# Optimization experiments

Hardware: AMD Instinct MI355X
Metric: run time of the kernel (lower is better)

The kernel has to match this reference:

```python
import jax, jax.numpy as jnp
import numpy as np

N, E, F_NODE, F_EDGE, H, L, G = 4096, 12288, 64, 16, 128, 4, 256
BN_EPS = 1e-5


def setup_inputs() -> dict:
    key = jax.random.key(0)
    ks = jax.random.split(key, 20)
    s = lambda k, shape, fan: jax.random.normal(k, shape, jnp.float32) * (1.0 / np.sqrt(fan))
    inp = {
        'x': jax.random.normal(ks[0], (N, F_NODE), jnp.float32),
        'edge_index': jax.random.randint(ks[1], (2, E), 0, N, dtype=jnp.int64),
        'edge_attr': jax.random.normal(ks[2], (E, F_EDGE), jnp.float32),
        'batch': jnp.sort(jax.random.randint(ks[3], (N,), 0, G, dtype=jnp.int64)),
        # node encoder
        'node_w': s(ks[4], (F_NODE, H), F_NODE),
        'node_b': jnp.zeros((H,), jnp.float32),
        # per-layer edge MLP: edge_feat -> 128 -> H*H
        'e1_w': s(ks[5], (L, F_EDGE, 128), F_EDGE),
        'e1_b': jnp.zeros((L, 128), jnp.float32),
        'e2_w': s(ks[6], (L, 128, H * H), 128) * 0.1,
        'e2_b': jnp.zeros((L, H * H), jnp.float32),
        # NNConv root weight + bias
        'root_w': s(ks[7], (L, H, H), H),
        'conv_b': jnp.zeros((L, H), jnp.float32),
        # batchnorm affine
        'bn_g': jnp.ones((L, H), jnp.float32),
        'bn_b': jnp.zeros((L, H), jnp.float32),
        # head
        'head_w1': s(ks[8], (H, H), H),
        'head_b1': jnp.zeros((H,), jnp.float32),
        'head_w2': s(ks[9], (H, 1), H),
        'head_b2': jnp.zeros((1,), jnp.float32),
    }
    return inp


def reference(x, edge_index, edge_attr, batch, node_w, node_b, e1_w, e1_b,
              e2_w, e2_b, root_w, conv_b, bn_g, bn_b, head_w1, head_b1,
              head_w2, head_b2):
    src, dst = edge_index[0], edge_index[1]
    h = x @ node_w + node_b  # [N,H]
    # in-degree for mean aggregation
    deg = jax.ops.segment_sum(jnp.ones((E,), h.dtype), dst, num_segments=N)
    inv_deg = jnp.where(deg > 0, 1.0 / jnp.maximum(deg, 1.0), 0.0)[:, None]
    for l in range(L):
        # edge MLP -> per-edge [H,H] weight
        e = jax.nn.relu(edge_attr @ e1_w[l] + e1_b[l])            # [E,128]
        W_e = (e @ e2_w[l] + e2_b[l]).reshape(E, H, H)            # [E,H,H]
        msg = jnp.einsum('eh,eho->eo', h[src], W_e)               # [E,H]
        agg = jax.ops.segment_sum(msg, dst, num_segments=N) * inv_deg
        out = agg + h @ root_w[l] + conv_b[l]
        # batchnorm (training-mode batch stats, biased var as in torch)
        mu = out.mean(0)
        var = out.var(0)
        out = (out - mu) * jax.lax.rsqrt(var + BN_EPS) * bn_g[l] + bn_b[l]
        h = h + jax.nn.relu(out)  # dropout disabled (eval)
    # global mean pool over graphs
    cnt = jax.ops.segment_sum(jnp.ones((N,), h.dtype), batch, num_segments=G)
    pooled = jax.ops.segment_sum(h, batch, num_segments=G) / jnp.maximum(cnt, 1.0)[:, None]
    y = jax.nn.relu(pooled @ head_w1 + head_b1) @ head_w2 + head_b2
    return y.squeeze(-1)  # [G]
```

## Files before the change

kernel.cpp:

```cpp
#include <hip/hip_runtime.h>

#define N_NODES 4096
#define E_TOT   12288
#define F_NODE  64
#define F_EDGE  16
#define HDIM    128
#define NLAYER  4
#define NGRAPH  256

typedef _Float16 half8 __attribute__((ext_vector_type(8)));
typedef float    f32x4 __attribute__((ext_vector_type(4)));

__global__ __launch_bounds__(256)
void k_prep_w2(const float* __restrict__ e2w, const float* __restrict__ e2b,
               _Float16* __restrict__ W2F)
{
    __shared__ _Float16 pg[16384];
    int b = blockIdx.x;
    int l = b / 129, k = b - l * 129;
    const float* src = (k < 128) ? (e2w + ((size_t)(l * 128 + k)) * 16384)
                                 : (e2b + (size_t)l * 16384);
    int t = threadIdx.x;
#pragma unroll
    for (int it = 0; it < 16; ++it) {
        int p = it * 1024 + t * 4;
        float4 v = *(const float4*)(src + p);
#pragma unroll
        for (int j4 = 0; j4 < 4; ++j4) {
            int p_ = p + j4;
            int h  = p_ >> 7, o = p_ & 127;
            int idx = ((h >> 5) * 8 + (o >> 4)) * 512
                    + (((h >> 3) & 3) * 16 + (o & 15)) * 8 + (h & 7);
            float val = (j4 == 0) ? v.x : (j4 == 1) ? v.y : (j4 == 2) ? v.z : v.w;
            pg[idx] = (_Float16)val;
        }
    }
    __syncthreads();
    _Float16* dst = W2F + (size_t)b * 16384;
#pragma unroll
    for (int it = 0; it < 8; ++it) {
        int i = it * 2048 + t * 8;
        *(half8*)(dst + i) = *(const half8*)(pg + i);
    }
}

__global__ __launch_bounds__(128)
void k_node_enc(const float* __restrict__ x, const float* __restrict__ nw,
                const float* __restrict__ nb, float* __restrict__ h,
                _Float16* __restrict__ hf)
{
    __shared__ float xl[F_NODE];
    int n = blockIdx.x, o = threadIdx.x;
    if (o < F_NODE) xl[o] = x[(size_t)n * F_NODE + o];
    __syncthreads();
    float acc = nb[o];
#pragma unroll 8
    for (int f = 0; f < F_NODE; ++f) acc += xl[f] * nw[f * HDIM + o];
    h [(size_t)n * HDIM + o] = acc;
    hf[(size_t)n * HDIM + o] = (_Float16)acc;
}

__global__ void k_deg(const int* __restrict__ dst, int* __restrict__ deg)
{
    int e = blockIdx.x * 256 + threadIdx.x;
    if (e < E_TOT) atomicAdd(&deg[dst[e]], 1);
}

__global__ void k_invd(const int* __restrict__ deg, float* __restrict__ invd)
{
    int n = blockIdx.x * 256 + threadIdx.x;
    if (n < N_NODES) invd[n] = deg[n] > 0 ? 1.0f / (float)deg[n] : 0.0f;
}

#define EF_STRIDE 136
__global__ __launch_bounds__(256)
void k_edge_mlp(const float* __restrict__ ea, const float* __restrict__ w1,
                const float* __restrict__ b1, _Float16* __restrict__ efg)
{
    __shared__ float al[16][17];
    __shared__ float wl[16][HDIM];
    __shared__ float bl[HDIM];
    int t = threadIdx.x, e0 = blockIdx.x * 16;
    if (t < HDIM) bl[t] = b1[t];
    for (int i = t; i < F_EDGE * HDIM; i += 256) wl[i >> 7][i & 127] = w1[i];
    { int i = t; al[i >> 4][i & 15] = ea[(size_t)e0 * F_EDGE + i]; }
    __syncthreads();
    int e = t >> 4, og = t & 15;
    float acc[8];
#pragma unroll
    for (int j = 0; j < 8; ++j) acc[j] = bl[og * 8 + j];
#pragma unroll
    for (int f = 0; f < F_EDGE; ++f) {
        float a = al[e][f];
#pragma unroll
        for (int j = 0; j < 8; ++j) acc[j] += a * wl[f][og * 8 + j];
    }
    half8 o;
#pragma unroll
    for (int j = 0; j < 8; ++j) o[j] = (_Float16)fmaxf(acc[j], 0.f);
    *(half8*)&efg[(size_t)(e0 + e) * EF_STRIDE + og * 8] = o;
    if (og == 0) efg[(size_t)(e0 + e) * EF_STRIDE + 128] = (_Float16)1.0f;
}

#define BM 64
#define KSPLIT 4
__global__ __launch_bounds__(128, 3)
void k_msg(const _Float16* __restrict__ W2L,
           const _Float16* __restrict__ efg,
           const _Float16* __restrict__ hf,
           const int* __restrict__ srcIdx,
           const int* __restrict__ dstIdx,
           float* __restrict__ agg,
           float* __restrict__ bns1,
           float* __restrict__ bns2)
{
    __shared__ _Float16 efs[BM][40];

    const int tid  = threadIdx.x;
    const int lane = tid & 63;
    const int w    = tid >> 6;
    const int lhi  = lane >> 4;
    const int llo  = lane & 15;

    const int bx    = blockIdx.x;
    const int code  = bx & 7;
    const int ks    = code >> 1;
    const int chH   = code & 1;
    const int tile  = bx >> 3;
    const int e0    = tile * BM;
    const int kbase = (129 * ks) >> 2;
    const int kcnt  = ((129 * (ks + 1)) >> 2) - kbase;

    if (bx == 0 && tid < HDIM) { bns1[tid] = 0.f; bns2[tid] = 0.f; }

    for (int i = tid; i < BM * 5; i += 128) {
        int r = i / 5, c = i - r * 5;
        *(half8*)&efs[r][c * 8] =
            *(const half8*)(efg + (size_t)(e0 + r) * EF_STRIDE + kbase + c * 8);
    }

    half8 hs[4][4];
#pragma unroll
    for (int rf = 0; rf < 4; ++rf) {
        int s = srcIdx[e0 + rf * 16 + llo];
        const _Float16* hp = hf + (size_t)s * HDIM + lhi * 8;
#pragma unroll
        for (int hc = 0; hc < 4; ++hc)
            hs[rf][hc] = *(const half8*)(hp + hc * 32);
    }

    __syncthreads();

    const _Float16* bp = W2L + (size_t)kbase * 16384
                             + (size_t)(chH * 4 + w * 2) * 512 + lane * 8;

#define LDQ(d0, d1, kk, hc) do {                                            \
        const _Float16* p_ = bp + (size_t)(kk) * 16384 + (hc) * 4096;       \
        d0 = *(const half8*)(p_); d1 = *(const half8*)(p_ + 512);           \
    } while (0)

    half8 b00, b01, b10, b11, b20, b21, b30, b31;
    LDQ(b00, b01, 0, 0);
    LDQ(b10, b11, 0, 1);
    LDQ(b20, b21, 0, 2);
    LDQ(b30, b31, 0, 3);

    f32x4 acc[4][2];
#pragma unroll
    for (int rf = 0; rf < 4; ++rf)
#pragma unroll
        for (int cf = 0; cf < 2; ++cf)
#pragma unroll
            for (int d = 0; d < 4; ++d) acc[rf][cf][d] = 0.f;

    for (int kk = 0; kk < kcnt; ++kk) {
        const bool nx = (kk + 1 < kcnt);
        _Float16 efv[4];
#pragma unroll
        for (int rf = 0; rf < 4; ++rf) efv[rf] = efs[rf * 16 + llo][kk];

        __builtin_amdgcn_s_setprio(1);
#pragma unroll
        for (int rf = 0; rf < 4; ++rf) {
            half8 av = hs[rf][0] * efv[rf];
            acc[rf][0] = __builtin_amdgcn_mfma_f32_16x16x32_f16(av, b00, acc[rf][0], 0, 0, 0);
            acc[rf][1] = __builtin_amdgcn_mfma_f32_16x16x32_f16(av, b01, acc[rf][1], 0, 0, 0);
        }
        if (nx) LDQ(b00, b01, kk + 1, 0);

#pragma unroll
        for (int rf = 0; rf < 4; ++rf) {
            half8 av = hs[rf][1] * efv[rf];
            acc[rf][0] = __builtin_amdgcn_mfma_f32_16x16x32_f16(av, b10, acc[rf][0], 0, 0, 0);
            acc[rf][1] = __builtin_amdgcn_mfma_f32_16x16x32_f16(av, b11, acc[rf][1], 0, 0, 0);
        }
        if (nx) LDQ(b10, b11, kk + 1, 1);

#pragma unroll
        for (int rf = 0; rf < 4; ++rf) {
            half8 av = hs[rf][2] * efv[rf];
            acc[rf][0] = __builtin_amdgcn_mfma_f32_16x16x32_f16(av, b20, acc[rf][0], 0, 0, 0);
            acc[rf][1] = __builtin_amdgcn_mfma_f32_16x16x32_f16(av, b21, acc[rf][1], 0, 0, 0);
        }
        if (nx) LDQ(b20, b21, kk + 1, 2);

#pragma unroll
        for (int rf = 0; rf < 4; ++rf) {
            half8 av = hs[rf][3] * efv[rf];
            acc[rf][0] = __builtin_amdgcn_mfma_f32_16x16x32_f16(av, b30, acc[rf][0], 0, 0, 0);
            acc[rf][1] = __builtin_amdgcn_mfma_f32_16x16x32_f16(av, b31, acc[rf][1], 0, 0, 0);
        }
        __builtin_amdgcn_s_setprio(0);
        if (nx) LDQ(b30, b31, kk + 1, 3);
    }
#undef LDQ

#pragma unroll
    for (int rf = 0; rf < 4; ++rf) {
#pragma unroll
        for (int r = 0; r < 4; ++r) {
            int row = rf * 16 + lhi * 4 + r;
            int d   = dstIdx[e0 + row];
#pragma unroll
            for (int cf = 0; cf < 2; ++cf) {
                int o = chH * 64 + w * 32 + cf * 16 + llo;
                atomicAdd(&agg[(size_t)d * HDIM + o], acc[rf][cf][r]);
            }
        }
    }
}

__global__ __launch_bounds__(128)
void k_out(const float* __restrict__ agg, const float* __restrict__ invd,
           const float* __restrict__ h, const float* __restrict__ rw,
           const float* __restrict__ cb, float* __restrict__ outb,
           float* __restrict__ bns1, float* __restrict__ bns2)
{
    __shared__ float hl[16][HDIM];
    int n0 = blockIdx.x * 16, o = threadIdx.x;
    for (int r = 0; r < 16; ++r) hl[r][o] = h[(size_t)(n0 + r) * HDIM + o];
    __syncthreads();
    float acc[16];
    float cbv = cb[o];
#pragma unroll
    for (int r = 0; r < 16; ++r)
        acc[r] = agg[(size_t)(n0 + r) * HDIM + o] * invd[n0 + r] + cbv;
    for (int hh = 0; hh < HDIM; ++hh) {
        float wv = rw[hh * HDIM + o];
#pragma unroll
        for (int r = 0; r < 16; ++r) acc[r] += hl[r][hh] * wv;
    }
    float s1 = 0.f, s2 = 0.f;
#pragma unroll
    for (int r = 0; r < 16; ++r) {
        outb[(size_t)(n0 + r) * HDIM + o] = acc[r];
        s1 += acc[r];
        s2 += acc[r] * acc[r];
    }
    atomicAdd(&bns1[o], s1);
    atomicAdd(&bns2[o], s2);
}

__global__ void k_bn_apply(const float* __restrict__ outb, const float* __restrict__ bns1,
                           const float* __restrict__ bns2, const float* __restrict__ g,
                           const float* __restrict__ b, float* __restrict__ h,
                           _Float16* __restrict__ hf, float* __restrict__ agg,
                           const int* __restrict__ batch, float* __restrict__ pooled,
                           int* __restrict__ cnt, int last)
{
    int i = blockIdx.x * 256 + threadIdx.x;
    int o = i & (HDIM - 1);
    const float inv_n = 1.0f / (float)N_NODES;
    float m   = bns1[o] * inv_n;
    float var = bns2[o] * inv_n - m * m;
    float rs  = rsqrtf(var + 1e-5f);
    float v  = (outb[i] - m) * rs * g[o] + b[o];
    float hn = h[i] + fmaxf(v, 0.f);
    h[i]  = hn;
    hf[i] = (_Float16)hn;
    if (!last) {
        agg[i] = 0.f;
    } else {
        int n  = i >> 7;
        int gg = batch[n];
        atomicAdd(&pooled[(size_t)gg * HDIM + o], hn);
        if (o == 0) atomicAdd(&cnt[gg], 1);
    }
}

__global__ __launch_bounds__(128)
void k_head(const float* __restrict__ pooled, const int* __restrict__ cnt,
            const float* __restrict__ w1, const float* __restrict__ b1,
            const float* __restrict__ w2, const float* __restrict__ b2,
            float* __restrict__ y)
{
    __shared__ float pl[HDIM];
    __shared__ float red[HDIM];
    int g = blockIdx.x, o = threadIdx.x;
    float ic = 1.0f / (float)max(cnt[g], 1);
    pl[o] = pooled[(size_t)g * HDIM + o] * ic;
    __syncthreads();
    float t = b1[o];
#pragma unroll 8
    for (int hh = 0; hh < HDIM; ++hh) t += pl[hh] * w1[hh * HDIM + o];
    t = fmaxf(t, 0.f);
    red[o] = t * w2[o];
    __syncthreads();
    for (int s = 64; s > 0; s >>= 1) {
        if (o < s) red[o] += red[o + s];
        __syncthreads();
    }
    if (o == 0) y[g] = red[0] + b2[0];
}

extern "C" void kernel_launch(void* const* d_in, const int* in_sizes, int n_in,
                              void* d_out, int out_size, void* d_ws, size_t ws_size,
                              hipStream_t stream)
{
    const float* x      = (const float*)d_in[0];
    const int*   ei     = (const int*)  d_in[1];
    const float* ea     = (const float*)d_in[2];
    const int*   batch  = (const int*)  d_in[3];
    const float* node_w = (const float*)d_in[4];
    const float* node_b = (const float*)d_in[5];
    const float* e1w    = (const float*)d_in[6];
    const float* e1b    = (const float*)d_in[7];
    const float* e2w    = (const float*)d_in[8];
    const float* e2b    = (const float*)d_in[9];
    const float* rw     = (const float*)d_in[10];
    const float* cb     = (const float*)d_in[11];
    const float* bng    = (const float*)d_in[12];
    const float* bnb    = (const float*)d_in[13];
    const float* hw1    = (const float*)d_in[14];
    const float* hb1    = (const float*)d_in[15];
    const float* hw2    = (const float*)d_in[16];
    const float* hb2    = (const float*)d_in[17];
    float* y = (float*)d_out;

    char* ws = (char*)d_ws;
    _Float16* W2F  = (_Float16*)ws; ws += 16908288;
    float*    h    = (float*)ws;    ws += 2097152;
    _Float16* hf   = (_Float16*)ws; ws += 1048576;
    _Float16* efg  = (_Float16*)ws; ws += 3342336;
    float*    agg  = (float*)ws;    ws += 2097152;
    float*    bns1 = (float*)ws;    ws += 512;
    float*    bns2 = (float*)ws;    ws += 512;
    float*    outb = (float*)ws;    ws += 2097152;
    int*      deg  = (int*)ws;      ws += 16384;
    float*    invd = (float*)ws;    ws += 16384;
    float*    pooled = (float*)ws;  ws += 131072;
    int*      cnt  = (int*)ws;      ws += 1024;

    const int* src = ei;
    const int* dst = ei + E_TOT;

    k_prep_w2<<<NLAYER * 129, 256, 0, stream>>>(e2w, e2b, W2F);
    k_node_enc<<<N_NODES, 128, 0, stream>>>(x, node_w, node_b, h, hf);
    hipMemsetAsync(deg, 0, N_NODES * sizeof(int), stream);
    k_deg<<<(E_TOT + 255) / 256, 256, 0, stream>>>(dst, deg);
    k_invd<<<(N_NODES + 255) / 256, 256, 0, stream>>>(deg, invd);
    hipMemsetAsync(agg, 0, (size_t)N_NODES * HDIM * sizeof(float), stream);
    hipMemsetAsync(pooled, 0, (size_t)NGRAPH * HDIM * sizeof(float) + NGRAPH * sizeof(int), stream);

    for (int l = 0; l < NLAYER; ++l) {
        k_edge_mlp<<<E_TOT / 16, 256, 0, stream>>>(ea, e1w + l * F_EDGE * HDIM,
                                                   e1b + l * HDIM, efg);
        k_msg<<<(E_TOT / BM) * KSPLIT * 2, 128, 0, stream>>>(
            W2F + (size_t)l * 129 * 16384, efg, hf, src, dst, agg, bns1, bns2);
        k_out<<<N_NODES / 16, 128, 0, stream>>>(agg, invd, h,
                                                rw + l * HDIM * HDIM,
                                                cb + l * HDIM, outb, bns1, bns2);
        k_bn_apply<<<(N_NODES * HDIM) / 256, 256, 0, stream>>>(
            outb, bns1, bns2, bng + l * HDIM, bnb + l * HDIM, h, hf,
            agg, batch, pooled, cnt, (l == NLAYER - 1) ? 1 : 0);
    }

    k_head<<<NGRAPH, 128, 0, stream>>>(pooled, cnt, hw1, hb1, hw2, hb2, y);
}
```

Baseline: 421.1 us.

## Fuse edge MLP into message kernel and register-tile the root transform

The per-layer edge MLP kernel is removed. Each message block now computes its own slice of relu(edge_attr·W1+b1) into shared memory, so the fp16 efg buffer is no longer written and read back through global memory. k_msg blocks grow to 256 threads and cover all 128 output channels, so the edge tile and the h gathers are shared across both channel halves; the setprio hints are dropped. k_out is rewritten with a 4x4 register tile, vectorized loads and a shared-memory reduction of the BN statistics before the global atomics. The trade-off is repeated small W1 reads from global memory and extra ALU work inside the MFMA kernel.

```diff
diff --git a/kernel.cpp b/kernel.cpp
--- a/kernel.cpp
+++ b/kernel.cpp
@@ -72,41 +72,13 @@
     if (n < N_NODES) invd[n] = deg[n] > 0 ? 1.0f / (float)deg[n] : 0.0f;
 }
 
-#define EF_STRIDE 136
-__global__ __launch_bounds__(256)
-void k_edge_mlp(const float* __restrict__ ea, const float* __restrict__ w1,
-                const float* __restrict__ b1, _Float16* __restrict__ efg)
-{
-    __shared__ float al[16][17];
-    __shared__ float wl[16][HDIM];
-    __shared__ float bl[HDIM];
-    int t = threadIdx.x, e0 = blockIdx.x * 16;
-    if (t < HDIM) bl[t] = b1[t];
-    for (int i = t; i < F_EDGE * HDIM; i += 256) wl[i >> 7][i & 127] = w1[i];
-    { int i = t; al[i >> 4][i & 15] = ea[(size_t)e0 * F_EDGE + i]; }
-    __syncthreads();
-    int e = t >> 4, og = t & 15;
-    float acc[8];
-#pragma unroll
-    for (int j = 0; j < 8; ++j) acc[j] = bl[og * 8 + j];
-#pragma unroll
-    for (int f = 0; f < F_EDGE; ++f) {
-        float a = al[e][f];
-#pragma unroll
-        for (int j = 0; j < 8; ++j) acc[j] += a * wl[f][og * 8 + j];
-    }
-    half8 o;
-#pragma unroll
-    for (int j = 0; j < 8; ++j) o[j] = (_Float16)fmaxf(acc[j], 0.f);
-    *(half8*)&efg[(size_t)(e0 + e) * EF_STRIDE + og * 8] = o;
-    if (og == 0) efg[(size_t)(e0 + e) * EF_STRIDE + 128] = (_Float16)1.0f;
-}
-
 #define BM 64
 #define KSPLIT 4
-__global__ __launch_bounds__(128, 3)
+__global__ __launch_bounds__(256, 3)
 void k_msg(const _Float16* __restrict__ W2L,
-           const _Float16* __restrict__ efg,
+           const float* __restrict__ ea,
+           const float* __restrict__ w1,
+           const float* __restrict__ b1,
            const _Float16* __restrict__ hf,
            const int* __restrict__ srcIdx,
            const int* __restrict__ dstIdx,
@@ -114,6 +86,7 @@
            float* __restrict__ bns1,
            float* __restrict__ bns2)
 {
+    __shared__ float    al[BM][17];
     __shared__ _Float16 efs[BM][40];
 
     const int tid  = threadIdx.x;
@@ -123,20 +96,21 @@
     const int llo  = lane & 15;
 
     const int bx    = blockIdx.x;
-    const int code  = bx & 7;
-    const int ks    = code >> 1;
-    const int chH   = code & 1;
-    const int tile  = bx >> 3;
+    const int ks    = (bx & 7) >> 1;
+    const int tile  = (bx >> 3) * 2 + (bx & 1);
     const int e0    = tile * BM;
     const int kbase = (129 * ks) >> 2;
     const int kcnt  = ((129 * (ks + 1)) >> 2) - kbase;
 
     if (bx == 0 && tid < HDIM) { bns1[tid] = 0.f; bns2[tid] = 0.f; }
 
-    for (int i = tid; i < BM * 5; i += 128) {
-        int r = i / 5, c = i - r * 5;
-        *(half8*)&efs[r][c * 8] =
-            *(const half8*)(efg + (size_t)(e0 + r) * EF_STRIDE + kbase + c * 8);
+    {
+        int e = tid >> 2, f0 = (tid & 3) * 4;
+        const float* p = ea + (size_t)(e0 + e) * F_EDGE + f0;
+        al[e][f0 + 0] = p[0];
+        al[e][f0 + 1] = p[1];
+        al[e][f0 + 2] = p[2];
+        al[e][f0 + 3] = p[3];
     }
 
     half8 hs[4][4];
@@ -151,8 +125,28 @@
 
     __syncthreads();
 
-    const _Float16* bp = W2L + (size_t)kbase * 16384
-                             + (size_t)(chH * 4 + w * 2) * 512 + lane * 8;
+    {
+        int e = tid >> 2, q = tid & 3;
+        int c0 = q * 9;
+        int c1 = c0 + 9 < kcnt ? c0 + 9 : kcnt;
+        for (int c = c0; c < c1; ++c) {
+            int kg = kbase + c;
+            float a;
+            if (kg == 128) {
+                a = 1.0f;
+            } else {
+                a = b1[kg];
+#pragma unroll
+                for (int f = 0; f < F_EDGE; ++f) a += al[e][f] * w1[f * HDIM + kg];
+                a = fmaxf(a, 0.f);
+            }
+            efs[e][c] = (_Float16)a;
+        }
+    }
+
+    __syncthreads();
+
+    const _Float16* bp = W2L + (size_t)kbase * 16384 + (w * 2) * 512 + lane * 8;
 
 #define LDQ(d0, d1, kk, hc) do {                                            \
         const _Float16* p_ = bp + (size_t)(kk) * 16384 + (hc) * 4096;       \
@@ -179,7 +173,6 @@
 #pragma unroll
         for (int rf = 0; rf < 4; ++rf) efv[rf] = efs[rf * 16 + llo][kk];
 
-        __builtin_amdgcn_s_setprio(1);
 #pragma unroll
         for (int rf = 0; rf < 4; ++rf) {
             half8 av = hs[rf][0] * efv[rf];
@@ -210,7 +203,6 @@
             acc[rf][0] = __builtin_amdgcn_mfma_f32_16x16x32_f16(av, b30, acc[rf][0], 0, 0, 0);
             acc[rf][1] = __builtin_amdgcn_mfma_f32_16x16x32_f16(av, b31, acc[rf][1], 0, 0, 0);
         }
-        __builtin_amdgcn_s_setprio(0);
         if (nx) LDQ(b30, b31, kk + 1, 3);
     }
 #undef LDQ
@@ -223,7 +215,7 @@
             int d   = dstIdx[e0 + row];
 #pragma unroll
             for (int cf = 0; cf < 2; ++cf) {
-                int o = chH * 64 + w * 32 + cf * 16 + llo;
+                int o = w * 32 + cf * 16 + llo;
                 atomicAdd(&agg[(size_t)d * HDIM + o], acc[rf][cf][r]);
             }
         }
@@ -236,29 +228,50 @@
            const float* __restrict__ cb, float* __restrict__ outb,
            float* __restrict__ bns1, float* __restrict__ bns2)
 {
-    __shared__ float hl[16][HDIM];
-    int n0 = blockIdx.x * 16, o = threadIdx.x;
-    for (int r = 0; r < 16; ++r) hl[r][o] = h[(size_t)(n0 + r) * HDIM + o];
-    __syncthreads();
-    float acc[16];
-    float cbv = cb[o];
-#pragma unroll
-    for (int r = 0; r < 16; ++r)
-        acc[r] = agg[(size_t)(n0 + r) * HDIM + o] * invd[n0 + r] + cbv;
-    for (int hh = 0; hh < HDIM; ++hh) {
-        float wv = rw[hh * HDIM + o];
-#pragma unroll
-        for (int r = 0; r < 16; ++r) acc[r] += hl[r][hh] * wv;
-    }
-    float s1 = 0.f, s2 = 0.f;
-#pragma unroll
-    for (int r = 0; r < 16; ++r) {
-        outb[(size_t)(n0 + r) * HDIM + o] = acc[r];
-        s1 += acc[r];
-        s2 += acc[r] * acc[r];
-    }
-    atomicAdd(&bns1[o], s1);
-    atomicAdd(&bns2[o], s2);
+    __shared__ float hl[16][132];
+    __shared__ float rb1[128], rb2[128];
+    int t = threadIdx.x, n0 = blockIdx.x * 16;
+    int rg = t >> 5, cg = t & 31;
+    for (int i = t; i < 16 * HDIM; i += 128)
+        hl[i >> 7][i & 127] = h[(size_t)(n0 + (i >> 7)) * HDIM + (i & 127)];
+    rb1[t] = 0.f; rb2[t] = 0.f;
+    __syncthreads();
+
+    f32x4 cbv = *(const f32x4*)&cb[cg * 4];
+    f32x4 acc[4];
+#pragma unroll
+    for (int i = 0; i < 4; ++i) {
+        int r = n0 + rg * 4 + i;
+        f32x4 a = *(const f32x4*)&agg[(size_t)r * HDIM + cg * 4];
+        acc[i] = a * invd[r] + cbv;
+    }
+    for (int hh = 0; hh < HDIM; hh += 4) {
+        f32x4 wv[4], hv[4];
+#pragma unroll
+        for (int j = 0; j < 4; ++j) wv[j] = *(const f32x4*)&rw[(hh + j) * HDIM + cg * 4];
+#pragma unroll
+        for (int i = 0; i < 4; ++i) hv[i] = *(const f32x4*)&hl[rg * 4 + i][hh];
+#pragma unroll
+        for (int i = 0; i < 4; ++i)
+#pragma unroll
+            for (int j = 0; j < 4; ++j)
+                acc[i] += hv[i][j] * wv[j];
+    }
+    f32x4 s1v = {0.f,0.f,0.f,0.f}, s2v = {0.f,0.f,0.f,0.f};
+#pragma unroll
+    for (int i = 0; i < 4; ++i) {
+        *(f32x4*)&outb[(size_t)(n0 + rg * 4 + i) * HDIM + cg * 4] = acc[i];
+        s1v += acc[i];
+        s2v += acc[i] * acc[i];
+    }
+#pragma unroll
+    for (int j = 0; j < 4; ++j) {
+        atomicAdd(&rb1[cg * 4 + j], s1v[j]);
+        atomicAdd(&rb2[cg * 4 + j], s2v[j]);
+    }
+    __syncthreads();
+    atomicAdd(&bns1[t], rb1[t]);
+    atomicAdd(&bns2[t], rb2[t]);
 }
 
 __global__ void k_bn_apply(const float* __restrict__ outb, const float* __restrict__ bns1,
@@ -341,7 +354,6 @@
     _Float16* W2F  = (_Float16*)ws; ws += 16908288;
     float*    h    = (float*)ws;    ws += 2097152;
     _Float16* hf   = (_Float16*)ws; ws += 1048576;
-    _Float16* efg  = (_Float16*)ws; ws += 3342336;
     float*    agg  = (float*)ws;    ws += 2097152;
     float*    bns1 = (float*)ws;    ws += 512;
     float*    bns2 = (float*)ws;    ws += 512;
@@ -363,10 +375,10 @@
     hipMemsetAsync(pooled, 0, (size_t)NGRAPH * HDIM * sizeof(float) + NGRAPH * sizeof(int), stream);
 
     for (int l = 0; l < NLAYER; ++l) {
-        k_edge_mlp<<<E_TOT / 16, 256, 0, stream>>>(ea, e1w + l * F_EDGE * HDIM,
-                                                   e1b + l * HDIM, efg);
-        k_msg<<<(E_TOT / BM) * KSPLIT * 2, 128, 0, stream>>>(
-            W2F + (size_t)l * 129 * 16384, efg, hf, src, dst, agg, bns1, bns2);
+        k_msg<<<(E_TOT / BM) * KSPLIT, 256, 0, stream>>>(
+            W2F + (size_t)l * 129 * 16384, ea,
+            e1w + l * F_EDGE * HDIM, e1b + l * HDIM,
+            hf, src, dst, agg, bns1, bns2);
         k_out<<<N_NODES / 16, 128, 0, stream>>>(agg, invd, h,
                                                 rw + l * HDIM * HDIM,
                                                 cb + l * HDIM, outb, bns1, bns2);
```

Result: slower. 431.6 us (+2.5%).
